# Performance work log

Hardware: AMD Instinct MI355X
Metric: run time of the kernel (lower is better)

The kernel has to match this reference:

```python
import jax, jax.numpy as jnp
import numpy as np
from math import pi

N = 256        # in_features == out_features
BATCH = 131072


def givens_orthogonal(angles, n):
    """Build an n x n orthogonal matrix as the ordered product of Givens
    rotations G(i, j, theta_k) over pairs i < j in lexicographic order.
    Each rotation mixes rows i and j; applied sequentially via lax.scan."""
    ii, jj = np.triu_indices(n, 1)  # static pair order, len = n*(n-1)//2
    ii = jnp.asarray(ii, dtype=jnp.int32)
    jj = jnp.asarray(jj, dtype=jnp.int32)

    def body(M, t):
        i, j, th = t
        c, s = jnp.cos(th), jnp.sin(th)
        ri, rj = M[i], M[j]
        M = M.at[i].set(c * ri - s * rj)
        M = M.at[j].set(s * ri + c * rj)
        return M, None

    M0 = jnp.eye(n, dtype=angles.dtype)
    M, _ = jax.lax.scan(body, M0, (ii, jj, angles))
    return M


def setup_inputs() -> dict:
    key = jax.random.key(0)
    k1, k2, k3 = jax.random.split(key, 3)
    n_ang = N * (N - 1) // 2  # 32640
    return {
        "x": jax.random.normal(k1, (BATCH, N), dtype=jnp.float32),
        "Uweight": jax.random.uniform(k2, (n_ang,), minval=-pi / 2, maxval=pi / 2, dtype=jnp.float32),
        "Vweight": jax.random.uniform(k3, (n_ang,), minval=-pi / 2, maxval=pi / 2, dtype=jnp.float32),
        "Sweight": jnp.ones((N,), dtype=jnp.float32),
        "bias": jnp.zeros((N,), dtype=jnp.float32),
    }


def reference(x, Uweight, Vweight, Sweight, bias):
    # W = V @ diag(S) @ U^T  (SVD-parametrized weight, out x in)
    # y = x @ W^T + b = ((x @ U) * S) @ V^T + b   (square case in == out)
    U = givens_orthogonal(Uweight, N)  # (in, in) orthogonal
    V = givens_orthogonal(Vweight, N)  # (out, out) orthogonal
    return ((x @ U) * Sweight) @ V.T + bias
```

## Files before the change

### kernel.cpp

```cpp
#include <hip/hip_runtime.h>
#include <hip/hip_bf16.h>
#include <math.h>

#define NN 256
#define NPAIR 32640
#define NSEG 32
#define MAT (NN*NN)

#define MATS0 0
#define MATS1 (MATS0 + 64*MAT)
#define WBT_OFF (MATS1 + 32*MAT)

static __device__ const int BD[NSEG+1] =
    {0,4,8,12,16,20,24,28,32,37,42,47,52,57,62,67,73,79,85,91,97,
     104,111,118,126,134,143,153,164,177,192,213,255};
#define CSL_CAP 1120

typedef __attribute__((ext_vector_type(8))) short short8;
typedef __attribute__((ext_vector_type(4))) float f32x4;

__device__ __forceinline__ short f2bf(float f) {
    __hip_bfloat16 h = __float2bfloat16(f);
    return *reinterpret_cast<short*>(&h);
}

#define BAR() do {                                              \
    asm volatile("s_waitcnt lgkmcnt(0)" ::: "memory");          \
    __builtin_amdgcn_s_barrier();                               \
    asm volatile("" ::: "memory");                              \
} while (0)

__global__ __launch_bounds__(64) void k_build(const float* __restrict__ au,
                                              const float* __restrict__ av,
                                              float* __restrict__ mats) {
    int b = blockIdx.x;
    int matid = b >> 7;
    int seg   = (b >> 2) & 31;
    int chunk = b & 3;
    int t = threadIdx.x;
    int c0 = chunk * 64;
    int i0 = BD[seg], i1 = BD[seg+1];
    float* outp = mats + (matid * NSEG + seg) * MAT;

    if (c0 + 64 <= i0) {
        for (int id = t; id < 4096; id += 64) {
            int row = id >> 4, c4 = (id & 15) * 4;
            float4 v = {0.f,0.f,0.f,0.f};
            int d = row - (c0 + c4);
            if (d >= 0 && d < 4) ((float*)&v)[d] = 1.0f;
            *(float4*)(outp + row*NN + c0 + c4) = v;
        }
        return;
    }

    __shared__ float M[NN * 64];
    __shared__ float2 csl[CSL_CAP];

    int kbase = 255*i0 - (i0*(i0-1))/2;
    int kend  = 255*i1 - (i1*(i1-1))/2;
    int nrot  = kend - kbase;
    const float* ang = (matid ? av : au) + kbase;
    for (int idx = t; idx < nrot; idx += 64) {
        float s, c;
        sincosf(ang[idx], &s, &c);
        float2 v = {c, s};
        csl[idx] = v;
    }

    int MR = NN - i0;
    for (int rr = 0; rr < MR; ++rr)
        M[rr*64 + t] = (i0 + rr == c0 + t) ? 1.0f : 0.0f;
    __syncthreads();

    for (int i = i0; i < i1; ++i) {
        int jstart = (i + 1 > c0) ? (i + 1) : c0;
        int kl = 255*i - (i*(i-1))/2 + (jstart - i - 1) - kbase;
        float ri = M[(i - i0)*64 + t];
        int j = jstart;
        int ng = (NN - jstart) >> 3;

        float2 cb[8]; float rj[8];
        if (ng > 0) {
#pragma unroll
            for (int u = 0; u < 8; ++u) cb[u] = csl[kl + u];
#pragma unroll
            for (int u = 0; u < 8; ++u) rj[u] = M[(j - i0 + u)*64 + t];
        }
        for (int g = 0; g < ng; ++g) {
            float2 cn[8]; float rn[8];
            if (g + 1 < ng) {
#pragma unroll
                for (int u = 0; u < 8; ++u) cn[u] = csl[kl + 8 + u];
#pragma unroll
                for (int u = 0; u < 8; ++u) rn[u] = M[(j + 8 - i0 + u)*64 + t];
            }
#pragma unroll
            for (int u = 0; u < 8; ++u) {
                float wv = cb[u].y*ri + cb[u].x*rj[u];
                ri       = cb[u].x*ri - cb[u].y*rj[u];
                M[(j - i0 + u)*64 + t] = wv;
            }
#pragma unroll
            for (int u = 0; u < 8; ++u) { cb[u] = cn[u]; rj[u] = rn[u]; }
            j += 8; kl += 8;
        }
        int rem = NN - j;
        if (rem > 0) {
            float2 cc[7]; float r7[7];
#pragma unroll
            for (int u = 0; u < 7; ++u)
                if (u < rem) { cc[u] = csl[kl + u];
                               r7[u] = M[(j - i0 + u)*64 + t]; }
#pragma unroll
            for (int u = 0; u < 7; ++u)
                if (u < rem) {
                    float wv = cc[u].y*ri + cc[u].x*r7[u];
                    ri       = cc[u].x*ri - cc[u].y*r7[u];
                    M[(j - i0 + u)*64 + t] = wv;
                }
        }
        M[(i - i0)*64 + t] = ri;
    }
    __syncthreads();

    for (int id = t; id < 4096; id += 64) {
        int row = id >> 4, c4 = (id & 15) * 4;
        float4 v;
        if (row < i0) {
            v = make_float4(0.f,0.f,0.f,0.f);
            int d = row - (c0 + c4);
            if (d >= 0 && d < 4) ((float*)&v)[d] = 1.0f;
        } else {
            v = *(const float4*)&M[(row - i0)*64 + c4];
        }
        *(float4*)(outp + row*NN + c0 + c4) = v;
    }
}

__global__ __launch_bounds__(256) void k_fold(const float* __restrict__ in,
                                              float* __restrict__ out,
                                              int nOut, int lg, int span) {
    int b = blockIdx.x;
    int np2 = 2 * nOut;
    int m    = b & (np2 - 1);
    int tile = b >> lg;
    int side = (m >= nOut) ? 1 : 0;
    int q = m - side * nOut;
    const float* A = in + (side*np2 + 2*q + 1) * MAT;
    const float* B = in + (side*np2 + 2*q) * MAT;
    float* C = out + m * MAT;
    int i0A = BD[q * span + (span >> 1)];
    int r0 = (tile >> 2) * 64, c0 = (tile & 3) * 64;
    int t = threadIdx.x;

    if (r0 + 64 <= i0A) {
#pragma unroll
        for (int u = 0; u < 4; ++u) {
            int id = u*256 + t;
            int rr = id >> 4, cc = (id & 15) * 4;
            *(float4*)(C + (r0+rr)*NN + c0 + cc) =
                *(const float4*)(B + (r0+rr)*NN + c0 + cc);
        }
        return;
    }

    int kstart = ((r0 < i0A) ? r0 : i0A) & ~31;
    int nt = (NN - kstart) >> 5;

    __shared__ float Ast[2][32][68];
    __shared__ float Bs [2][32][68];
    int tx = t & 15, ty = t >> 4;
    int arow = t >> 3, ak4 = t & 7;
    int bkr = t >> 4, bc4 = t & 15;

    float acc[4][4] = {};
    f32x4 pa0, pa1, pb0, pb1;
    {
        int kt = kstart;
        pa0 = *(const f32x4*)(A + (r0 + arow     )*NN + kt + ak4*4);
        pa1 = *(const f32x4*)(A + (r0 + arow + 32)*NN + kt + ak4*4);
        pb0 = *(const f32x4*)(B + (kt + bkr      )*NN + c0 + bc4*4);
        pb1 = *(const f32x4*)(B + (kt + bkr + 16 )*NN + c0 + bc4*4);
    }
    for (int it = 0; it < nt; ++it) {
        int cur = it & 1;
#pragma unroll
        for (int jj = 0; jj < 4; ++jj) {
            Ast[cur][ak4*4 + jj][arow]      = pa0[jj];
            Ast[cur][ak4*4 + jj][arow + 32] = pa1[jj];
        }
        *(f32x4*)&Bs[cur][bkr     ][bc4*4] = pb0;
        *(f32x4*)&Bs[cur][bkr + 16][bc4*4] = pb1;
        if (it + 1 < nt) {
            int k2 = kstart + (it+1)*32;
            pa0 = *(const f32x4*)(A + (r0 + arow     )*NN + k2 + ak4*4);
            pa1 = *(const f32x4*)(A + (r0 + arow + 32)*NN + k2 + ak4*4);
            pb0 = *(const f32x4*)(B + (k2 + bkr      )*NN + c0 + bc4*4);
            pb1 = *(const f32x4*)(B + (k2 + bkr + 16 )*NN + c0 + bc4*4);
        }
        BAR();
#pragma unroll 8
        for (int kk = 0; kk < 32; ++kk) {
            f32x4 a4 = *(const f32x4*)&Ast[cur][kk][ty*4];
            f32x4 b4 = *(const f32x4*)&Bs [cur][kk][tx*4];
#pragma unroll
            for (int rr = 0; rr < 4; ++rr)
#pragma unroll
                for (int cc = 0; cc < 4; ++cc)
                    acc[rr][cc] = fmaf(a4[rr], b4[cc], acc[rr][cc]);
        }
    }
#pragma unroll
    for (int rr = 0; rr < 4; ++rr) {
        float4 o = {acc[rr][0], acc[rr][1], acc[rr][2], acc[rr][3]};
        *(float4*)(C + (r0 + ty*4 + rr)*NN + c0 + tx*4) = o;
    }
}

__global__ __launch_bounds__(256) void k_wmatT(const float* __restrict__ U,
                                               const float* __restrict__ V,
                                               const float* __restrict__ S,
                                               unsigned short* __restrict__ Wbt) {
    int b = blockIdx.x;
    int n0 = (b >> 4) * 16, i0 = (b & 15) * 16;
    int t = threadIdx.x, ti = t & 15, tn = t >> 4;
    __shared__ float Us[16][260];
    __shared__ float Vs[16][260];
    {
        int rr = t >> 4, cc = (t & 15) * 16;
#pragma unroll
        for (int q = 0; q < 4; ++q) {
            float4 u = *(const float4*)(U + (i0+rr)*NN + cc + q*4);
            float4 s = *(const float4*)(S + cc + q*4);
            u.x *= s.x; u.y *= s.y; u.z *= s.z; u.w *= s.w;
            *(float4*)&Us[rr][cc+q*4] = u;
            *(float4*)&Vs[rr][cc+q*4] = *(const float4*)(V + (n0+rr)*NN + cc + q*4);
        }
    }
    __syncthreads();
    float acc = 0.f;
#pragma unroll 8
    for (int k4 = 0; k4 < 64; ++k4) {
        float4 uu = *(const float4*)&Us[ti][k4*4];
        float4 vv = *(const float4*)&Vs[tn][k4*4];
        acc += uu.x*vv.x + uu.y*vv.y + uu.z*vv.z + uu.w*vv.w;
    }
    Wbt[(n0+tn)*NN + (i0+ti)] = (unsigned short)f2bf(acc);
}

__global__ __launch_bounds__(512, 4) void k_mm(const float* __restrict__ x,
                                               const unsigned short* __restrict__ Wbt,
                                               const float* __restrict__ bias,
                                               float* __restrict__ out) {
    int t = threadIdx.x;
    int w = t >> 6, l = t & 63, l15 = l & 15, lg = l >> 4;
    int n0 = w * 32;

    __shared__ unsigned short Xs[2][8 * 512];

    long row0 = (long)blockIdx.x * 64;
    int r = t & 15, m = t >> 4;
    int ksb = m >> 2;
    int lidx = r + 16 * (m & 3);

    const float* s0 = x + (row0 + r) * NN + 8*m;
    float4 f0 = *(const float4*)(s0);
    float4 f1 = *(const float4*)(s0 + 4);

    short8 bfrag[2][8];
#pragma unroll
    for (int nt = 0; nt < 2; ++nt) {
        const unsigned short* wrow = Wbt + (n0 + nt*16 + l15) * NN + lg * 8;
#pragma unroll
        for (int ks = 0; ks < 8; ++ks)
            bfrag[nt][ks] = *(const short8*)(wrow + ks * 32);
    }
    float b0 = bias[n0 + l15];
    float b1 = bias[n0 + 16 + l15];

#pragma unroll
    for (int it = 0; it < 4; ++it) {
        int cur = it & 1;
        short8 h;
        h[0]=f2bf(f0.x); h[1]=f2bf(f0.y); h[2]=f2bf(f0.z); h[3]=f2bf(f0.w);
        h[4]=f2bf(f1.x); h[5]=f2bf(f1.y); h[6]=f2bf(f1.z); h[7]=f2bf(f1.w);
        *(short8*)&Xs[cur][ksb*512 + lidx*8] = h;
        if (it < 3) {
            const float* sn = x + (row0 + (it+1)*16 + r) * NN + 8*m;
            f0 = *(const float4*)(sn);
            f1 = *(const float4*)(sn + 4);
        }
        BAR();

        f32x4 acc0 = {0.f,0.f,0.f,0.f}, acc1 = {0.f,0.f,0.f,0.f};
#pragma unroll
        for (int ks = 0; ks < 8; ++ks) {
            short8 af = *(const short8*)&Xs[cur][ks*512 + l*8];
            acc0 = __builtin_amdgcn_mfma_f32_16x16x32_bf16(af, bfrag[0][ks], acc0, 0, 0, 0);
            acc1 = __builtin_amdgcn_mfma_f32_16x16x32_bf16(af, bfrag[1][ks], acc1, 0, 0, 0);
        }
        float* op = out + (row0 + it*16 + lg*4) * NN + n0 + l15;
#pragma unroll
        for (int rr = 0; rr < 4; ++rr) {
            op[rr * NN]      = acc0[rr] + b0;
            op[rr * NN + 16] = acc1[rr] + b1;
        }
    }
}

extern "C" void kernel_launch(void* const* d_in, const int* in_sizes, int n_in,
                              void* d_out, int out_size, void* d_ws, size_t ws_size,
                              hipStream_t stream) {
    const float* x    = (const float*)d_in[0];
    const float* Uw   = (const float*)d_in[1];
    const float* Vw   = (const float*)d_in[2];
    const float* Sw   = (const float*)d_in[3];
    const float* bias = (const float*)d_in[4];
    float* out = (float*)d_out;
    float* ws  = (float*)d_ws;

    k_build<<<256, 64, 0, stream>>>(Uw, Vw, ws + MATS0);
    k_fold<<<16*32, 256, 0, stream>>>(ws + MATS0, ws + MATS1, 16, 5, 2);
    k_fold<<<16*16, 256, 0, stream>>>(ws + MATS1, ws + MATS0,  8, 4, 4);
    k_fold<<<16* 8, 256, 0, stream>>>(ws + MATS0, ws + MATS1,  4, 3, 8);
    k_fold<<<16* 4, 256, 0, stream>>>(ws + MATS1, ws + MATS0,  2, 2, 16);
    k_fold<<<16* 2, 256, 0, stream>>>(ws + MATS0, ws + MATS1,  1, 1, 32);
    k_wmatT<<<256, 256, 0, stream>>>(ws + MATS1, ws + MATS1 + MAT, Sw,
                                     (unsigned short*)(ws + WBT_OFF));
    k_mm<<<2048, 512, 0, stream>>>(x, (unsigned short*)(ws + WBT_OFF), bias, out);
}
```

Baseline: 215.8 us.

## Fuse weight-prep kernels into one persistent launch with grid barriers; enlarge GEMM blocks

Replaces the build, five fold launches and the W-transpose launch with one persistent 512-block kernel. The stages are separated by atomic-counter grid barriers in workspace, which is zeroed by a memset before the launch. This is meant to remove per-launch overhead and tail gaps between the small prep kernels. The main GEMM now handles 256 rows per block across 512 blocks instead of 64 rows across 2048, which amortizes the B-fragment loads. The risks are a deadlock if all 512 blocks are not co-resident, idle blocks spinning in the later stages, and fewer GEMM blocks to fill the CUs.

New measurement: 646.1 us. 199% more time.

```diff
diff --git a/kernel.cpp b/kernel.cpp
--- a/kernel.cpp
+++ b/kernel.cpp
@@ -3,13 +3,13 @@
 #include <math.h>
 
 #define NN 256
-#define NPAIR 32640
 #define NSEG 32
 #define MAT (NN*NN)
 
 #define MATS0 0
 #define MATS1 (MATS0 + 64*MAT)
 #define WBT_OFF (MATS1 + 32*MAT)
+#define BAR_OFF (WBT_OFF + 32768)
 
 static __device__ const int BD[NSEG+1] =
     {0,4,8,12,16,20,24,28,32,37,42,47,52,57,62,67,73,79,85,91,97,
@@ -30,14 +30,31 @@
     asm volatile("" ::: "memory");                              \
 } while (0)
 
-__global__ __launch_bounds__(64) void k_build(const float* __restrict__ au,
-                                              const float* __restrict__ av,
-                                              float* __restrict__ mats) {
-    int b = blockIdx.x;
+#define WAVE_LDS_FENCE() asm volatile("s_waitcnt lgkmcnt(0)" ::: "memory")
+
+#define PREP_GRID 512
+
+__device__ __forceinline__ void gridbar(unsigned* cnt, int id) {
+    __syncthreads();
+    if (threadIdx.x == 0) {
+        __threadfence();
+        __hip_atomic_fetch_add(&cnt[id], 1u, __ATOMIC_RELEASE,
+                               __HIP_MEMORY_SCOPE_AGENT);
+        while (__hip_atomic_load(&cnt[id], __ATOMIC_ACQUIRE,
+                                 __HIP_MEMORY_SCOPE_AGENT) < PREP_GRID)
+            __builtin_amdgcn_s_sleep(16);
+        __threadfence();
+    }
+    __syncthreads();
+}
+
+__device__ __forceinline__ void build_seg(const float* __restrict__ au,
+                                          const float* __restrict__ av,
+                                          float* __restrict__ mats,
+                                          int b, int t, unsigned char* smem) {
     int matid = b >> 7;
     int seg   = (b >> 2) & 31;
     int chunk = b & 3;
-    int t = threadIdx.x;
     int c0 = chunk * 64;
     int i0 = BD[seg], i1 = BD[seg+1];
     float* outp = mats + (matid * NSEG + seg) * MAT;
@@ -53,8 +70,8 @@
         return;
     }
 
-    __shared__ float M[NN * 64];
-    __shared__ float2 csl[CSL_CAP];
+    float*  M   = (float*)smem;
+    float2* csl = (float2*)(smem + 65536);
 
     int kbase = 255*i0 - (i0*(i0-1))/2;
     int kend  = 255*i1 - (i1*(i1-1))/2;
@@ -66,11 +83,10 @@
         float2 v = {c, s};
         csl[idx] = v;
     }
-
     int MR = NN - i0;
     for (int rr = 0; rr < MR; ++rr)
         M[rr*64 + t] = (i0 + rr == c0 + t) ? 1.0f : 0.0f;
-    __syncthreads();
+    WAVE_LDS_FENCE();
 
     for (int i = i0; i < i1; ++i) {
         int jstart = (i + 1 > c0) ? (i + 1) : c0;
@@ -121,7 +137,7 @@
         }
         M[(i - i0)*64 + t] = ri;
     }
-    __syncthreads();
+    WAVE_LDS_FENCE();
 
     for (int id = t; id < 4096; id += 64) {
         int row = id >> 4, c4 = (id & 15) * 4;
@@ -137,10 +153,10 @@
     }
 }
 
-__global__ __launch_bounds__(256) void k_fold(const float* __restrict__ in,
-                                              float* __restrict__ out,
-                                              int nOut, int lg, int span) {
-    int b = blockIdx.x;
+__device__ __forceinline__ void fold_unit(const float* __restrict__ in,
+                                          float* __restrict__ out,
+                                          int nOut, int lg, int span,
+                                          int b, int t, unsigned char* smem) {
     int np2 = 2 * nOut;
     int m    = b & (np2 - 1);
     int tile = b >> lg;
@@ -151,7 +167,6 @@
     float* C = out + m * MAT;
     int i0A = BD[q * span + (span >> 1)];
     int r0 = (tile >> 2) * 64, c0 = (tile & 3) * 64;
-    int t = threadIdx.x;
 
     if (r0 + 64 <= i0A) {
 #pragma unroll
@@ -167,8 +182,8 @@
     int kstart = ((r0 < i0A) ? r0 : i0A) & ~31;
     int nt = (NN - kstart) >> 5;
 
-    __shared__ float Ast[2][32][68];
-    __shared__ float Bs [2][32][68];
+    float (*Ast)[32][68] = (float(*)[32][68])smem;
+    float (*Bs )[32][68] = (float(*)[32][68])(smem + 17408);
     int tx = t & 15, ty = t >> 4;
     int arow = t >> 3, ak4 = t & 7;
     int bkr = t >> 4, bc4 = t & 15;
@@ -217,15 +232,15 @@
     }
 }
 
-__global__ __launch_bounds__(256) void k_wmatT(const float* __restrict__ U,
-                                               const float* __restrict__ V,
-                                               const float* __restrict__ S,
-                                               unsigned short* __restrict__ Wbt) {
-    int b = blockIdx.x;
+__device__ __forceinline__ void wmatT_unit(const float* __restrict__ U,
+                                           const float* __restrict__ V,
+                                           const float* __restrict__ S,
+                                           unsigned short* __restrict__ Wbt,
+                                           int b, int t, unsigned char* smem) {
     int n0 = (b >> 4) * 16, i0 = (b & 15) * 16;
-    int t = threadIdx.x, ti = t & 15, tn = t >> 4;
-    __shared__ float Us[16][260];
-    __shared__ float Vs[16][260];
+    int ti = t & 15, tn = t >> 4;
+    float (*Us)[260] = (float(*)[260])smem;
+    float (*Vs)[260] = (float(*)[260])(smem + 16640);
     {
         int rr = t >> 4, cc = (t & 15) * 16;
 #pragma unroll
@@ -248,6 +263,30 @@
     Wbt[(n0+tn)*NN + (i0+ti)] = (unsigned short)f2bf(acc);
 }
 
+__global__ __launch_bounds__(256, 2)
+void k_prep(const float* __restrict__ au, const float* __restrict__ av,
+            const float* __restrict__ S, float* __restrict__ ws,
+            unsigned short* __restrict__ Wbt, unsigned* __restrict__ cnt) {
+    __shared__ __align__(16) unsigned char smem[74496];
+    int b = blockIdx.x, t = threadIdx.x;
+    float* m0 = ws + MATS0;
+    float* m1 = ws + MATS1;
+
+    if (b < 256 && t < 64) build_seg(au, av, m0, b, t, smem);
+    gridbar(cnt, 0);
+    fold_unit(m0, m1, 16, 5,  2, b, t, smem);
+    gridbar(cnt, 1);
+    if (b < 256) fold_unit(m1, m0,  8, 4,  4, b, t, smem);
+    gridbar(cnt, 2);
+    if (b < 128) fold_unit(m0, m1,  4, 3,  8, b, t, smem);
+    gridbar(cnt, 3);
+    if (b <  64) fold_unit(m1, m0,  2, 2, 16, b, t, smem);
+    gridbar(cnt, 4);
+    if (b <  32) fold_unit(m0, m1,  1, 1, 32, b, t, smem);
+    gridbar(cnt, 5);
+    if (b < 256) wmatT_unit(m1, m1 + MAT, S, Wbt, b, t, smem);
+}
+
 __global__ __launch_bounds__(512, 4) void k_mm(const float* __restrict__ x,
                                                const unsigned short* __restrict__ Wbt,
                                                const float* __restrict__ bias,
@@ -258,12 +297,12 @@
 
     __shared__ unsigned short Xs[2][8 * 512];
 
-    long row0 = (long)blockIdx.x * 64;
+    long rowbase = (long)blockIdx.x * 256;
     int r = t & 15, m = t >> 4;
     int ksb = m >> 2;
     int lidx = r + 16 * (m & 3);
 
-    const float* s0 = x + (row0 + r) * NN + 8*m;
+    const float* s0 = x + (rowbase + r) * NN + 8*m;
     float4 f0 = *(const float4*)(s0);
     float4 f1 = *(const float4*)(s0 + 4);
 
@@ -278,15 +317,14 @@
     float b0 = bias[n0 + l15];
     float b1 = bias[n0 + 16 + l15];
 
-#pragma unroll
-    for (int it = 0; it < 4; ++it) {
+    for (int it = 0; it < 16; ++it) {
         int cur = it & 1;
         short8 h;
         h[0]=f2bf(f0.x); h[1]=f2bf(f0.y); h[2]=f2bf(f0.z); h[3]=f2bf(f0.w);
         h[4]=f2bf(f1.x); h[5]=f2bf(f1.y); h[6]=f2bf(f1.z); h[7]=f2bf(f1.w);
         *(short8*)&Xs[cur][ksb*512 + lidx*8] = h;
-        if (it < 3) {
-            const float* sn = x + (row0 + (it+1)*16 + r) * NN + 8*m;
+        if (it < 15) {
+            const float* sn = x + (rowbase + (it+1)*16 + r) * NN + 8*m;
             f0 = *(const float4*)(sn);
             f1 = *(const float4*)(sn + 4);
         }
@@ -299,7 +337,7 @@
             acc0 = __builtin_amdgcn_mfma_f32_16x16x32_bf16(af, bfrag[0][ks], acc0, 0, 0, 0);
             acc1 = __builtin_amdgcn_mfma_f32_16x16x32_bf16(af, bfrag[1][ks], acc1, 0, 0, 0);
         }
-        float* op = out + (row0 + it*16 + lg*4) * NN + n0 + l15;
+        float* op = out + (rowbase + it*16 + lg*4) * NN + n0 + l15;
 #pragma unroll
         for (int rr = 0; rr < 4; ++rr) {
             op[rr * NN]      = acc0[rr] + b0;
@@ -319,13 +357,9 @@
     float* out = (float*)d_out;
     float* ws  = (float*)d_ws;
 
-    k_build<<<256, 64, 0, stream>>>(Uw, Vw, ws + MATS0);
-    k_fold<<<16*32, 256, 0, stream>>>(ws + MATS0, ws + MATS1, 16, 5, 2);
-    k_fold<<<16*16, 256, 0, stream>>>(ws + MATS1, ws + MATS0,  8, 4, 4);
-    k_fold<<<16* 8, 256, 0, stream>>>(ws + MATS0, ws + MATS1,  4, 3, 8);
-    k_fold<<<16* 4, 256, 0, stream>>>(ws + MATS1, ws + MATS0,  2, 2, 16);
-    k_fold<<<16* 2, 256, 0, stream>>>(ws + MATS0, ws + MATS1,  1, 1, 32);
-    k_wmatT<<<256, 256, 0, stream>>>(ws + MATS1, ws + MATS1 + MAT, Sw,
-                                     (unsigned short*)(ws + WBT_OFF));
-    k_mm<<<2048, 512, 0, stream>>>(x, (unsigned short*)(ws + WBT_OFF), bias, out);
-}
+    hipMemsetAsync(ws + BAR_OFF, 0, 64, stream);
+    k_prep<<<PREP_GRID, 256, 0, stream>>>(Uw, Vw, Sw, ws,
+                                          (unsigned short*)(ws + WBT_OFF),
+                                          (unsigned*)(ws + BAR_OFF));
+    k_mm<<<512, 512, 0, stream>>>(x, (unsigned short*)(ws + WBT_OFF), bias, out);
+}
```
